# Optimization experiments

Measured on AMD Instinct MI355X. Metric: run time of the kernel, lower is better.

## Reference

```python
import jax, jax.numpy as jnp
import numpy as np

HEADS = 8
DIM_HEAD = 32
HTK = 576
WTK = 576


def layernorm(x, g, b, eps=1e-6):
    mu = x.mean(-1, keepdims=True)
    var = ((x - mu) ** 2).mean(-1, keepdims=True)
    return (x - mu) * jax.lax.rsqrt(var + eps) * g + b


def conv2d(x, w, b, pad, groups=1):
    y = jax.lax.conv_general_dilated(
        x, w, (1, 1), [(pad, pad), (pad, pad)],
        dimension_numbers=('NCHW', 'OIHW', 'NCHW'),
        feature_group_count=groups)
    return y + b[None, :, None, None]


def prune_attn(attn, htk, wtk):
    B, H, N, _ = attn.shape
    bi = jnp.arange(B)[:, None, None]
    hi = jnp.arange(H)[None, :, None]
    # row pruning: score rows by mean over keys, keep top-k rows
    row_scores = attn.mean(-1)                       # [B,H,N]
    _, top_row = jax.lax.top_k(row_scores, htk)      # [B,H,htk]
    row_mask = jnp.zeros((B, H, N), attn.dtype).at[bi, hi, top_row].set(1.0)
    # col pruning: score cols by mean over queries, keep top-k cols
    col_scores = attn.mean(-2)                       # [B,H,N]
    _, top_col = jax.lax.top_k(col_scores, wtk)
    col_mask = jnp.zeros((B, H, N), attn.dtype).at[bi, hi, top_col].set(1.0)
    return attn * row_mask[..., :, None] * col_mask[..., None, :]


def setup_inputs() -> dict:
    key = jax.random.key(0)
    ks = jax.random.split(key, 24)
    C = 256
    hid = C * 4
    g = C // 8
    s = 0.02
    inp = {
        'x': jax.random.normal(ks[0], (2, C, 48, 48), jnp.float32),
        'qkv_w': jax.random.normal(ks[1], (C, 3 * C), jnp.float32) * s,
        'out_w': jax.random.normal(ks[2], (C, C), jnp.float32) * s,
        'ln1_g': jnp.ones((C,), jnp.float32),
        'ln1_b': jnp.zeros((C,), jnp.float32),
        'ln2_g': jnp.ones((C,), jnp.float32),
        'ln2_b': jnp.zeros((C,), jnp.float32),
        'dw_w': jax.random.normal(ks[3], (C, 1, 3, 3), jnp.float32) * s,
        'dw_b': jnp.zeros((C,), jnp.float32),
        'pw_w': jax.random.normal(ks[4], (C, C, 1, 1), jnp.float32) * s,
        'pw_b': jnp.zeros((C,), jnp.float32),
        'sg1_w': jax.random.normal(ks[5], (g, C, 1, 1), jnp.float32) * s,
        'sg1_b': jnp.zeros((g,), jnp.float32),
        'sg2_w': jax.random.normal(ks[6], (1, g, 7, 7), jnp.float32) * s,
        'sg2_b': jnp.zeros((1,), jnp.float32),
        'cg1_w': jax.random.normal(ks[7], (g, C, 1, 1), jnp.float32) * s,
        'cg1_b': jnp.zeros((g,), jnp.float32),
        'cg2_w': jax.random.normal(ks[8], (C, g, 1, 1), jnp.float32) * s,
        'cg2_b': jnp.zeros((C,), jnp.float32),
        'ff_w1': jax.random.normal(ks[9], (C, hid), jnp.float32) * s,
        'ff_b1': jnp.zeros((hid,), jnp.float32),
        'ff_w2': jax.random.normal(ks[10], (hid, C), jnp.float32) * s,
        'ff_b2': jnp.zeros((C,), jnp.float32),
        'gamma1': jnp.full((1,), 0.5, jnp.float32),
        'gamma2': jnp.full((1,), 0.5, jnp.float32),
    }
    return inp


def reference(x, qkv_w, out_w, ln1_g, ln1_b, ln2_g, ln2_b, dw_w, dw_b,
              pw_w, pw_b, sg1_w, sg1_b, sg2_w, sg2_b, cg1_w, cg1_b,
              cg2_w, cg2_b, ff_w1, ff_b1, ff_w2, ff_b2, gamma1, gamma2):
    B, C, H, W = x.shape
    N = H * W
    # ---- dual-pruned self-attention branch ----
    xa = x.transpose(0, 2, 3, 1).reshape(B, N, C)
    xa = layernorm(xa, ln1_g, ln1_b)
    qkv = xa @ qkv_w                                    # [B,N,3C]
    q, k, v = jnp.split(qkv, 3, axis=-1)
    rs = lambda t: t.reshape(B, N, HEADS, DIM_HEAD).transpose(0, 2, 1, 3)
    q, k, v = rs(q), rs(k), rs(v)                       # [B,h,N,d]
    attn = jnp.einsum('bhid,bhjd->bhij', q, k) * (DIM_HEAD ** -0.5)
    attn = prune_attn(attn, HTK, WTK)
    attn = jax.nn.softmax(attn, axis=-1)
    o = jnp.einsum('bhij,bhjd->bhid', attn, v)
    o = o.transpose(0, 2, 1, 3).reshape(B, N, C) @ out_w
    x_attn = o.reshape(B, H, W, C).transpose(0, 3, 1, 2)
    # ---- conv branch ----
    xc = conv2d(x, dw_w, dw_b, pad=1, groups=C)
    xc = conv2d(xc, pw_w, pw_b, pad=0)
    xs = x_attn + xc
    # ---- gates ----
    sg = jax.nn.silu(conv2d(xs, sg1_w, sg1_b, pad=0))
    sg = jax.nn.sigmoid(conv2d(sg, sg2_w, sg2_b, pad=3))   # [B,1,H,W]
    cg = xs.mean(axis=(2, 3), keepdims=True)                # [B,C,1,1]
    cg = jax.nn.silu(conv2d(cg, cg1_w, cg1_b, pad=0))
    cg = jax.nn.sigmoid(conv2d(cg, cg2_w, cg2_b, pad=0))
    x2 = x + gamma1[0] * (xs * sg * cg)
    # ---- FFN ----
    normed = layernorm(x2.transpose(0, 2, 3, 1), ln2_g, ln2_b)
    h = jax.nn.gelu(normed @ ff_w1 + ff_b1, approximate=False)
    ff = (h @ ff_w2 + ff_b2).transpose(0, 3, 1, 2)
    return x2 + gamma2[0] * ff
```

## Files before the change

kernel.cpp:

```cpp
#include <hip/hip_runtime.h>
#include <math.h>

#define N_PIX 2304
#define CCH   256
#define BHN   16
#define KTOP  576
#define NROWS 4608

typedef unsigned short u16;
typedef __attribute__((ext_vector_type(8))) short short8v;
typedef __attribute__((ext_vector_type(4))) float floatx4;

__device__ __forceinline__ u16 f2b(float f) {
  unsigned int u = __float_as_uint(f);
  return (u16)((u + 0x7fffu + ((u >> 16) & 1u)) >> 16);
}
__device__ __forceinline__ float b2f(u16 v) {
  return __uint_as_float(((unsigned int)v) << 16);
}

__device__ __forceinline__ void async16(const void* g, void* l) {
  __builtin_amdgcn_global_load_lds(
      (const __attribute__((address_space(1))) unsigned int*)g,
      (__attribute__((address_space(3))) unsigned int*)l, 16, 0, 0);
}

__device__ __forceinline__ float erf_apx(float x) {
  float ax = fabsf(x);
  float u = 1.f / (1.f + 0.3275911f * ax);
  float y = u * (0.254829592f + u * (-0.284496736f + u * (1.421413741f +
            u * (-1.453152027f + u * 1.061405429f))));
  float r = 1.f - y * expf(-ax * ax);
  return (x < 0.f) ? -r : r;
}

__global__ __launch_bounds__(256) void lncast_kernel(
    const float* __restrict__ x, u16* __restrict__ xa_bf, float* __restrict__ xnhwc,
    const float* __restrict__ g, const float* __restrict__ beta,
    const float* __restrict__ qkv_w, const float* __restrict__ out_w,
    const float* __restrict__ pw_w, const float* __restrict__ ff_w1,
    const float* __restrict__ ff_w2, const float* __restrict__ sg1_w,
    u16* __restrict__ qkvBT, u16* __restrict__ B2,
    u16* __restrict__ ff1BT, u16* __restrict__ ff2BT, u16* __restrict__ sg1BT)
{
  __shared__ float tile[32 * 257];
  __shared__ float redS[8 * 32], redQ[8 * 32];
  __shared__ float mu_s[32], rs_s[32];
  int tid = threadIdx.x;
  if (blockIdx.x >= 144) {
    int i = (blockIdx.x - 144) * 256 + tid;
    if (i < 196608) { int k = i / 768, n = i - k * 768; qkvBT[n * 256 + k] = f2b(qkv_w[i]); return; }
    i -= 196608;
    if (i < 65536) { int k = i >> 8, n = i & 255; B2[n * 512 + k] = f2b(out_w[i]); return; }
    i -= 65536;
    if (i < 65536) { int n = i >> 8, ic = i & 255; B2[n * 512 + 256 + ic] = f2b(pw_w[i]); return; }
    i -= 65536;
    if (i < 262144) { int k = i >> 10, n = i & 1023; ff1BT[n * 256 + k] = f2b(ff_w1[i]); return; }
    i -= 262144;
    if (i < 262144) { int k = i & 1023, n = i >> 10; ff2BT[i] = f2b(ff_w2[k * 256 + n]); return; }
    i -= 262144;
    if (i < 16384) sg1BT[i] = (i < 8192) ? f2b(sg1_w[i]) : (u16)0;
    return;
  }
  int p0g = blockIdx.x * 32;
  int bb = p0g / N_PIX; int p0 = p0g - bb * N_PIX;
  int px = tid & 31, csub = tid >> 5;
  float sacc = 0.f, qacc = 0.f;
#pragma unroll 4
  for (int it = 0; it < 32; ++it) {
    int c = it * 8 + csub;
    float v = x[((long)bb * 256 + c) * N_PIX + p0 + px];
    tile[px * 257 + c] = v;
    sacc += v; qacc += v * v;
  }
  redS[csub * 32 + px] = sacc; redQ[csub * 32 + px] = qacc;
  __syncthreads();
  if (tid < 32) {
    float s = 0.f, qq = 0.f;
#pragma unroll
    for (int j = 0; j < 8; ++j) { s += redS[j * 32 + tid]; qq += redQ[j * 32 + tid]; }
    float mu = s * (1.f / 256.f);
    float var = qq * (1.f / 256.f) - mu * mu;
    mu_s[tid] = mu; rs_s[tid] = rsqrtf(var + 1e-6f);
  }
  __syncthreads();
  float gv = g[tid], bv = beta[tid];
#pragma unroll 4
  for (int it = 0; it < 32; ++it) {
    float v = tile[it * 257 + tid];
    long orow = (long)(p0g + it) * 256 + tid;
    xnhwc[orow] = v;
    xa_bf[orow] = f2b((v - mu_s[it]) * rs_s[it] * gv + bv);
  }
}

template<int MT, int EPI, int CS>
__global__ __launch_bounds__(256) void mgemm(
    const u16* __restrict__ A, const u16* __restrict__ BT,
    float* __restrict__ C, u16* __restrict__ C2,
    int K, int ldc, int nvalid,
    const float* __restrict__ bias, const float* __restrict__ add,
    const float* __restrict__ gamma,
    float* __restrict__ cs_out, int cs_ld,
    const u16* __restrict__ xs2, const float* __restrict__ sgv,
    const float* __restrict__ cgv, const float* __restrict__ g1p)
{
  __shared__ u16 Als[MT * 64 * 32];
  __shared__ u16 Bls[64 * 32];
  int tid = threadIdx.x;
  int w = tid >> 6, lane = tid & 63;
  int row0 = blockIdx.y * (MT * 64), col0 = blockIdx.x * 64;
  const u16* Abase = A + (long)row0 * K;
  const u16* Bbase = BT + (long)col0 * K;
  int q = lane >> 4, l15 = lane & 15;

  floatx4 acc[MT][4];
#pragma unroll
  for (int mi = 0; mi < MT; ++mi)
#pragma unroll
    for (int ni = 0; ni < 4; ++ni) acc[mi][ni] = (floatx4)0.f;

  int ccB = w * 64 + lane;
  int rB = ccB >> 2, kB = (ccB & 3) << 3;

  for (int k0 = 0; k0 < K; k0 += 32) {
#pragma unroll
    for (int i = 0; i < MT; ++i) {
      int cc = w * (64 * MT) + i * 64 + lane;
      async16(Abase + (long)(cc >> 2) * K + k0 + ((cc & 3) << 3), &Als[cc * 8]);
    }
    async16(Bbase + (long)rB * K + k0 + kB, &Bls[ccB * 8]);
    __syncthreads();
    short8v a[MT];
#pragma unroll
    for (int mi = 0; mi < MT; ++mi)
      a[mi] = *(const short8v*)&Als[(w * (16 * MT) + mi * 16 + l15) * 32 + q * 8];
#pragma unroll
    for (int ni = 0; ni < 4; ++ni) {
      short8v b = *(const short8v*)&Bls[(ni * 16 + l15) * 32 + q * 8];
#pragma unroll
      for (int mi = 0; mi < MT; ++mi)
        acc[mi][ni] = __builtin_amdgcn_mfma_f32_16x16x32_bf16(a[mi], b, acc[mi][ni], 0, 0, 0);
    }
    __syncthreads();
  }

  float g2 = (EPI == 5) ? gamma[0] : 0.f;
  float g1v = (EPI == 5) ? g1p[0] : 0.f;
  float cp[4] = {0.f, 0.f, 0.f, 0.f};
#pragma unroll
  for (int mi = 0; mi < MT; ++mi) {
#pragma unroll
    for (int ni = 0; ni < 4; ++ni) {
      int c = col0 + ni * 16 + l15;
      int rbase = row0 + w * (16 * MT) + mi * 16 + q * 4;
#pragma unroll
      for (int reg = 0; reg < 4; ++reg) {
        long row = rbase + reg;
        float v = acc[mi][ni][reg];
        if (EPI == 0) {
          C[row * ldc + c] = v;
          if (CS) cp[ni] += v;
        } else if (EPI == 3) {
          if (c < nvalid) {
            float t = v + bias[c];
            C[row * (long)nvalid + c] = t / (1.f + expf(-t));
          }
        } else if (EPI == 4) {
          float t = v + bias[c];
          t = 0.5f * t * (1.f + erf_apx(t * 0.70710678f));
          C2[row * ldc + c] = f2b(t);
        } else if (EPI == 5) {
          int bb = (int)(row / N_PIX); int p = (int)(row - (long)bb * N_PIX);
          float xsv = b2f(xs2[row * 256 + c]);
          float x2v = add[row * 256 + c] + g1v * xsv * sgv[row] * cgv[bb * 256 + c];
          float t = x2v + g2 * (v + bias[c]);
          C[((long)bb * 256 + c) * N_PIX + p] = t;
        } else if (EPI == 7) {
          float t = v + bias[c];
          C2[row * ldc + c] = f2b(t);
          if (CS) cp[ni] += t;
        }
      }
    }
  }
  if (CS) {
    int bb = (row0 >= N_PIX) ? 1 : 0;
#pragma unroll
    for (int ni = 0; ni < 4; ++ni) {
      float r = cp[ni];
      r += __shfl_xor(r, 16);
      r += __shfl_xor(r, 32);
      if (lane < 16) atomicAdd(&cs_out[bb * cs_ld + col0 + ni * 16 + l15], r);
    }
  }
}

__global__ __launch_bounds__(256) void topkscore_kernel(
    const float* __restrict__ qkv, const float* __restrict__ csum, int* __restrict__ out_idx)
{
  int bh = blockIdx.x, which = blockIdx.y;
  int b = bh >> 3, h = bh & 7;
  int* out = out_idx + (which * BHN + bh) * KTOP;
  __shared__ unsigned int u[N_PIX];
  __shared__ unsigned int hist[256];
  __shared__ unsigned int wtmp[4];
  __shared__ unsigned int sh_selbin, sh_selS;
  __shared__ unsigned int cnt_eq[4], cnt_sel[4];
  __shared__ float svl[32];
  int tid = threadIdx.x;
  int wave = tid >> 6, lane = tid & 63;
  unsigned long long ltmask = (1ull << lane) - 1ull;
  if (tid < 32) svl[tid] = csum[b * 768 + (which ? 0 : 256) + h * 32 + tid];
  __syncthreads();
  int off = (which ? 256 : 0) + h * 32;
  for (int i = tid; i < N_PIX; i += 256) {
    const float4* p4 = (const float4*)(qkv + ((long)(b * N_PIX + i)) * 768 + off);
    float sc = 0.f;
#pragma unroll
    for (int j = 0; j < 8; ++j) {
      float4 v = p4[j];
      sc += v.x * svl[j * 4] + v.y * svl[j * 4 + 1] + v.z * svl[j * 4 + 2] + v.w * svl[j * 4 + 3];
    }
    unsigned int bu = __float_as_uint(sc);
    u[i] = (bu & 0x80000000u) ? ~bu : (bu | 0x80000000u);
  }
  __syncthreads();
  unsigned int prefix = 0u, kRem = KTOP;
  for (int pass = 0; pass < 4; ++pass) {
    int shift = 24 - pass * 8;
    hist[tid] = 0u;
    __syncthreads();
    unsigned int mask = (pass == 0) ? 0u : (0xFFFFFFFFu << (shift + 8));
    for (int i = tid; i < N_PIX; i += 256) {
      unsigned int v = u[i];
      if ((v & mask) == prefix) atomicAdd(&hist[(v >> shift) & 255u], 1u);
    }
    __syncthreads();
    int v = (int)hist[255 - tid];
    int xsc = v;
#pragma unroll
    for (int o = 1; o < 64; o <<= 1) { int y = __shfl_up(xsc, o); if (lane >= o) xsc += y; }
    if (lane == 63) wtmp[wave] = (unsigned int)xsc;
    __syncthreads();
    int wadd = 0;
    for (int ww = 0; ww < wave; ++ww) wadd += (int)wtmp[ww];
    unsigned int S = (unsigned int)(xsc + wadd - v);
    if (S < kRem && S + (unsigned int)v >= kRem) { sh_selbin = (unsigned int)(255 - tid); sh_selS = S; }
    __syncthreads();
    prefix |= (sh_selbin << shift);
    kRem -= sh_selS;
    __syncthreads();
  }
  unsigned int T = prefix;
  unsigned int run_sel = 0u, run_eq = 0u;
  for (int c0 = 0; c0 < N_PIX; c0 += 256) {
    int i = c0 + tid;
    unsigned int v = u[i];
    bool isGt = v > T, isEq = (v == T);
    unsigned long long be = __ballot(isEq);
    unsigned int eqpre = (unsigned int)__popcll(be & ltmask);
    if (lane == 0) cnt_eq[wave] = (unsigned int)__popcll(be);
    __syncthreads();
    unsigned int eqoff = run_eq + eqpre;
    for (int ww = 0; ww < wave; ++ww) eqoff += cnt_eq[ww];
    bool selF = isGt || (isEq && eqoff < kRem);
    unsigned long long bs = __ballot(selF);
    unsigned int spre = (unsigned int)__popcll(bs & ltmask);
    if (lane == 0) cnt_sel[wave] = (unsigned int)__popcll(bs);
    __syncthreads();
    unsigned int soff = run_sel + spre;
    for (int ww = 0; ww < wave; ++ww) soff += cnt_sel[ww];
    if (selF) out[soff] = i;
    unsigned int te = 0, ts = 0;
#pragma unroll
    for (int ww = 0; ww < 4; ++ww) { te += cnt_eq[ww]; ts += cnt_sel[ww]; }
    run_eq += te; run_sel += ts;
    __syncthreads();
  }
}

__global__ __launch_bounds__(256) void gather_kernel(
    const float* __restrict__ qkv, const int* __restrict__ idx,
    u16* __restrict__ Qg, u16* __restrict__ Kg, u16* __restrict__ VgT,
    float* __restrict__ vneg, const float* __restrict__ csum, u16* __restrict__ A2)
{
  __shared__ float red[256];
  int bh = blockIdx.y;
  int tid = threadIdx.x;
  int r = blockIdx.x * 8 + (tid >> 5);
  int d = tid & 31;
  int b = bh >> 3, h = bh & 7;
  int rn = idx[bh * KTOP + r];
  int cn = idx[(BHN + bh) * KTOP + r];
  const float scale = 0.17677669529663687f;
  float vv = qkv[((long)(b * N_PIX + cn)) * 768 + 512 + h * 32 + d];
  Qg [((long)bh * KTOP + r) * 32 + d] = f2b(qkv[((long)(b * N_PIX + rn)) * 768 + h * 32 + d] * scale);
  Kg [((long)bh * KTOP + r) * 32 + d] = f2b(qkv[((long)(b * N_PIX + cn)) * 768 + 256 + h * 32 + d]);
  VgT[((long)bh * 32 + d) * 584 + r] = f2b(vv);
  red[tid] = vv;
  int bid = blockIdx.y * 72 + blockIdx.x;
  int row = 4 * bid + (tid >> 6);
  int b2 = row / N_PIX;
  int c4 = (tid & 63) * 4;
  const float* vm = csum + b2 * 768 + 512 + c4;
  ushort4 ov;
  ov.x = f2b(vm[0] * (1.f / (float)N_PIX));
  ov.y = f2b(vm[1] * (1.f / (float)N_PIX));
  ov.z = f2b(vm[2] * (1.f / (float)N_PIX));
  ov.w = f2b(vm[3] * (1.f / (float)N_PIX));
  *(ushort4*)&A2[(long)row * 512 + c4] = ov;
  __syncthreads();
  if (tid < 32) {
    float s = 0.f;
#pragma unroll
    for (int j = 0; j < 8; ++j) s += red[j * 32 + tid];
    atomicAdd(&vneg[bh * 32 + tid], s);
  }
}

__global__ __launch_bounds__(256) void attn_kernel(
    const u16* __restrict__ Qg, const u16* __restrict__ Kg, const u16* __restrict__ VgT,
    const float* __restrict__ csum, const float* __restrict__ vneg,
    const int* __restrict__ idx, u16* __restrict__ A2)
{
  __shared__ u16 Pls[32 * 584];
  __shared__ float wmax[4 * 32], wsum[4 * 32];
  __shared__ float emv_s[32], invd_s[32], vdif_s[32];
  int bh = blockIdx.y;
  int row0 = blockIdx.x * 32;
  int tid = threadIdx.x;
  int w = tid >> 6, lane = tid & 63;
  int q = lane >> 4, l15 = lane & 15;
  int b = bh >> 3, h = bh & 7;
  if (tid < 32) vdif_s[tid] = csum[b * 768 + 512 + h * 32 + tid] - vneg[bh * 32 + tid];
  const u16* Qb = Qg + (long)bh * KTOP * 32;
  const u16* Kb = Kg + (long)bh * KTOP * 32;
  short8v af[2];
#pragma unroll
  for (int mi = 0; mi < 2; ++mi)
    af[mi] = *(const short8v*)(Qb + ((long)(row0 + mi * 16 + l15)) * 32 + q * 8);
  floatx4 sacc[2][9];
#pragma unroll
  for (int mi = 0; mi < 2; ++mi)
#pragma unroll
    for (int ni = 0; ni < 9; ++ni) sacc[mi][ni] = (floatx4)0.f;
#pragma unroll
  for (int ni = 0; ni < 9; ++ni) {
    int n = w * 144 + ni * 16 + l15;
    short8v bf = *(const short8v*)(Kb + (long)n * 32 + q * 8);
#pragma unroll
    for (int mi = 0; mi < 2; ++mi)
      sacc[mi][ni] = __builtin_amdgcn_mfma_f32_16x16x32_bf16(af[mi], bf, sacc[mi][ni], 0, 0, 0);
  }
#pragma unroll
  for (int mi = 0; mi < 2; ++mi)
#pragma unroll
    for (int reg = 0; reg < 4; ++reg) {
      float m = sacc[mi][0][reg];
#pragma unroll
      for (int ni = 1; ni < 9; ++ni) m = fmaxf(m, sacc[mi][ni][reg]);
#pragma unroll
      for (int o = 1; o < 16; o <<= 1) m = fmaxf(m, __shfl_xor(m, o));
      if (l15 == 0) wmax[w * 32 + mi * 16 + q * 4 + reg] = m;
    }
  __syncthreads();
#pragma unroll
  for (int mi = 0; mi < 2; ++mi)
#pragma unroll
    for (int reg = 0; reg < 4; ++reg) {
      int r = mi * 16 + q * 4 + reg;
      float gm = fmaxf(fmaxf(fmaxf(wmax[r], wmax[32 + r]), fmaxf(wmax[64 + r], wmax[96 + r])), 0.f);
      float s = 0.f;
#pragma unroll
      for (int ni = 0; ni < 9; ++ni) {
        float e = expf(sacc[mi][ni][reg] - gm);
        s += e;
        Pls[r * 584 + w * 144 + ni * 16 + l15] = f2b(e);
      }
#pragma unroll
      for (int o = 1; o < 16; o <<= 1) s += __shfl_xor(s, o);
      if (l15 == 0) wsum[w * 32 + r] = s;
    }
  __syncthreads();
  if (tid < 32) {
    float gm = fmaxf(fmaxf(fmaxf(wmax[tid], wmax[32 + tid]), fmaxf(wmax[64 + tid], wmax[96 + tid])), 0.f);
    float s = wsum[tid] + wsum[32 + tid] + wsum[64 + tid] + wsum[96 + tid];
    float em = expf(-gm);
    float inv = 1.f / (s + (float)(N_PIX - KTOP) * em);
    invd_s[tid] = inv;
    emv_s[tid] = em * inv;
  }
  __syncthreads();
  int mw = w & 1, nw = w >> 1;
  const u16* Vb = VgT + (long)bh * 32 * 584;
  floatx4 acc = (floatx4)0.f;
#pragma unroll
  for (int kt = 0; kt < 18; ++kt) {
    int k0 = kt * 32;
    short8v a = *(const short8v*)&Pls[(mw * 16 + l15) * 584 + k0 + q * 8];
    short8v bb = *(const short8v*)(Vb + (long)(nw * 16 + l15) * 584 + k0 + q * 8);
    acc = __builtin_amdgcn_mfma_f32_16x16x32_bf16(a, bb, acc, 0, 0, 0);
  }
  int d = nw * 16 + l15;
  float vd = vdif_s[d];
#pragma unroll
  for (int reg = 0; reg < 4; ++reg) {
    int r = mw * 16 + q * 4 + reg;
    float o = acc[reg] * invd_s[r] + emv_s[r] * vd;
    int n = idx[bh * KTOP + row0 + r];
    A2[((long)(b * N_PIX + n)) * 512 + h * 32 + d] = f2b(o);
  }
}

__global__ __launch_bounds__(256) void dwconv_kernel(
    const float* __restrict__ xnhwc, const float* __restrict__ w,
    const float* __restrict__ bias, u16* __restrict__ A2)
{
  int pix = blockIdx.x;
  int b = pix / N_PIX; int p = pix - b * N_PIX;
  int y = p / 48, xx = p - y * 48;
  int c = threadIdx.x;
  float acc = bias[c];
#pragma unroll
  for (int ky = 0; ky < 3; ++ky) {
    int yy = y + ky - 1; if (yy < 0 || yy >= 48) continue;
#pragma unroll
    for (int kx = 0; kx < 3; ++kx) {
      int xc = xx + kx - 1; if (xc < 0 || xc >= 48) continue;
      acc += w[c * 9 + ky * 3 + kx] * xnhwc[((long)(b * N_PIX + yy * 48 + xc)) * 256 + c];
    }
  }
  A2[(long)pix * 512 + 256 + c] = f2b(acc);
}

__global__ __launch_bounds__(256) void sgcg_kernel(
    const float* __restrict__ sga, const float* __restrict__ w,
    const float* __restrict__ b1, float* __restrict__ sgate,
    const float* __restrict__ cgm, const float* __restrict__ cw1, const float* __restrict__ cb1,
    const float* __restrict__ cw2, const float* __restrict__ cb2, float* __restrict__ cgate)
{
  __shared__ float ws[32 * 49];
  __shared__ float red[4 * 64];
  __shared__ float m[256];
  __shared__ float a[32];
  int t = threadIdx.x;
  if (blockIdx.x >= 96) {
    int b = blockIdx.x - 96;
    m[t] = cgm[b * 256 + t] * (1.f / (float)N_PIX);
    __syncthreads();
    if (t < 32) {
      float s = cb1[t];
      for (int c = 0; c < 256; ++c) s += cw1[t * 256 + c] * m[c];
      a[t] = s / (1.f + expf(-s));
    }
    __syncthreads();
    float s = cb2[t];
#pragma unroll
    for (int g = 0; g < 32; ++g) s += cw2[t * 32 + g] * a[g];
    cgate[b * 256 + t] = 1.f / (1.f + expf(-s));
    return;
  }
  int by = blockIdx.x; int b = by / 48, y = by - b * 48;
  for (int i = t; i < 32 * 49; i += 256) ws[i] = w[i];
  __syncthreads();
  int xx = t & 63, gg = t >> 6;
  float acc = 0.f;
  if (xx < 48) {
    for (int ky = 0; ky < 7; ++ky) {
      int yy = y + ky - 3; if (yy < 0 || yy >= 48) continue;
      for (int kx = 0; kx < 7; ++kx) {
        int xc = xx + kx - 3; if (xc < 0 || xc >= 48) continue;
        const float4* sp = (const float4*)(sga + ((long)(b * N_PIX + yy * 48 + xc)) * 32 + gg * 8);
        float4 v0 = sp[0], v1 = sp[1];
        int wb = gg * 8 * 49 + ky * 7 + kx;
        acc += ws[wb] * v0.x + ws[wb + 49] * v0.y + ws[wb + 98] * v0.z + ws[wb + 147] * v0.w;
        acc += ws[wb + 196] * v1.x + ws[wb + 245] * v1.y + ws[wb + 294] * v1.z + ws[wb + 343] * v1.w;
      }
    }
  }
  red[gg * 64 + xx] = acc;
  __syncthreads();
  if (t < 48) {
    float tot = b1[0] + red[t] + red[64 + t] + red[128 + t] + red[192 + t];
    sgate[b * N_PIX + y * 48 + t] = 1.f / (1.f + expf(-tot));
  }
}

__global__ __launch_bounds__(256) void gln_kernel(
    const float* __restrict__ xnhwc, const u16* __restrict__ xs_bf,
    const float* __restrict__ sgate, const float* __restrict__ cgate,
    const float* __restrict__ gamma1,
    const float* __restrict__ g, const float* __restrict__ bvec, u16* __restrict__ normed)
{
  __shared__ float red[256];
  int pix = blockIdx.x; int b = pix / N_PIX;
  int c = threadIdx.x;
  float xsv = b2f(xs_bf[(long)pix * 256 + c]);
  float v = xnhwc[(long)pix * 256 + c] + gamma1[0] * xsv * sgate[pix] * cgate[b * 256 + c];
  red[c] = v; __syncthreads();
  for (int off = 128; off > 0; off >>= 1) { if (c < off) red[c] += red[c + off]; __syncthreads(); }
  float mu = red[0] * (1.f / 256.f);
  __syncthreads();
  float dv = v - mu;
  red[c] = dv * dv; __syncthreads();
  for (int off = 128; off > 0; off >>= 1) { if (c < off) red[c] += red[c + off]; __syncthreads(); }
  float var = red[0] * (1.f / 256.f);
  normed[(long)pix * 256 + c] = f2b(dv * rsqrtf(var + 1e-6f) * g[c] + bvec[c]);
}

extern "C" void kernel_launch(void* const* d_in, const int* in_sizes, int n_in,
                              void* d_out, int out_size, void* d_ws, size_t ws_size,
                              hipStream_t stream) {
  (void)in_sizes; (void)n_in; (void)out_size; (void)ws_size;
  const float* x      = (const float*)d_in[0];
  const float* qkv_w  = (const float*)d_in[1];
  const float* out_w  = (const float*)d_in[2];
  const float* ln1_g  = (const float*)d_in[3];
  const float* ln1_b  = (const float*)d_in[4];
  const float* ln2_g  = (const float*)d_in[5];
  const float* ln2_b  = (const float*)d_in[6];
  const float* dw_w   = (const float*)d_in[7];
  const float* dw_b   = (const float*)d_in[8];
  const float* pw_w   = (const float*)d_in[9];
  const float* pw_b   = (const float*)d_in[10];
  const float* sg1_w  = (const float*)d_in[11];
  const float* sg1_b  = (const float*)d_in[12];
  const float* sg2_w  = (const float*)d_in[13];
  const float* sg2_b  = (const float*)d_in[14];
  const float* cg1_w  = (const float*)d_in[15];
  const float* cg1_b  = (const float*)d_in[16];
  const float* cg2_w  = (const float*)d_in[17];
  const float* cg2_b  = (const float*)d_in[18];
  const float* ff_w1  = (const float*)d_in[19];
  const float* ff_b1  = (const float*)d_in[20];
  const float* ff_w2  = (const float*)d_in[21];
  const float* ff_b2  = (const float*)d_in[22];
  const float* gamma1 = (const float*)d_in[23];
  const float* gamma2 = (const float*)d_in[24];
  float* out = (float*)d_out;
  float* ws  = (float*)d_ws;

  float* qkv     = ws + 0;
  u16*   A2      = (u16*)(ws + 3538944);
  float* xnhwc   = ws + 4718592;
  u16*   xa_bf   = (u16*)(ws + 5898240);
  u16*   xs_bf   = (u16*)(ws + 6488064);
  u16*   Qg_bf   = (u16*)(ws + 7077888);
  u16*   Kg_bf   = (u16*)(ws + 7225344);
  u16*   VgT     = (u16*)(ws + 7372800);
  float* sga     = ws + 7522304;
  float* csum    = ws + 7669760;
  float* vneg    = ws + 7671296;
  float* cgm     = ws + 7671808;
  float* sgate   = ws + 7672320;
  float* cgate   = ws + 7676928;
  int*   idxb    = (int*)(ws + 7677440);
  u16*   qkvBT   = (u16*)(ws + 7695872);
  u16*   B2combo = (u16*)(ws + 7794176);
  u16*   ff1BT   = (u16*)(ws + 7859712);
  u16*   ff2BT   = (u16*)(ws + 7990784);
  u16*   sg1BT   = (u16*)(ws + 8121856);
  u16*   h_bf     = (u16*)qkv;
  u16*   normed_bf= (u16*)(ws + 2359296);

  dim3 blk(256);
  hipMemsetAsync(csum, 0, 2560 * sizeof(float), stream);

  lncast_kernel<<<dim3(3536), blk, 0, stream>>>(x, xa_bf, xnhwc, ln1_g, ln1_b,
      qkv_w, out_w, pw_w, ff_w1, ff_w2, sg1_w,
      qkvBT, B2combo, ff1BT, ff2BT, sg1BT);

  mgemm<2, 0, 1><<<dim3(12, 36), blk, 0, stream>>>(xa_bf, qkvBT, qkv, nullptr,
      256, 768, 768, nullptr, nullptr, nullptr, csum, 768, nullptr, nullptr, nullptr, nullptr);
  topkscore_kernel<<<dim3(BHN, 2), blk, 0, stream>>>(qkv, csum, idxb);
  gather_kernel<<<dim3(72, BHN), blk, 0, stream>>>(qkv, idxb, Qg_bf, Kg_bf, VgT, vneg,
      csum, A2);
  attn_kernel<<<dim3(18, BHN), blk, 0, stream>>>(Qg_bf, Kg_bf, VgT, csum, vneg, idxb, A2);

  dwconv_kernel<<<dim3(NROWS), blk, 0, stream>>>(xnhwc, dw_w, dw_b, A2);

  mgemm<1, 7, 1><<<dim3(4, 72), blk, 0, stream>>>(A2, B2combo, nullptr, xs_bf,
      512, 256, 256, pw_b, nullptr, nullptr, cgm, 256, nullptr, nullptr, nullptr, nullptr);

  mgemm<1, 3, 0><<<dim3(1, 72), blk, 0, stream>>>(xs_bf, sg1BT, sga, nullptr,
      256, 32, 32, sg1_b, nullptr, nullptr, nullptr, 0, nullptr, nullptr, nullptr, nullptr);
  sgcg_kernel<<<dim3(98), blk, 0, stream>>>(sga, sg2_w, sg2_b, sgate,
      cgm, cg1_w, cg1_b, cg2_w, cg2_b, cgate);

  gln_kernel<<<dim3(NROWS), blk, 0, stream>>>(xnhwc, xs_bf, sgate, cgate, gamma1,
      ln2_g, ln2_b, normed_bf);

  mgemm<2, 4, 0><<<dim3(16, 36), blk, 0, stream>>>(normed_bf, ff1BT, nullptr, h_bf,
      256, 1024, 1024, ff_b1, nullptr, nullptr, nullptr, 0, nullptr, nullptr, nullptr, nullptr);
  mgemm<1, 5, 0><<<dim3(4, 72), blk, 0, stream>>>(h_bf, ff2BT, out, nullptr,
      1024, 256, 256, ff_b2, xnhwc, gamma2, nullptr, 0, xs_bf, sgate, cgate, gamma1);
}
```

Baseline: 256.7 us.

## Load GEMM operands directly to registers; fuse dwconv into topk; fold memset

The GEMM drops its LDS staging and barriers, so each wave loads its A and B MFMA fragments straight from global memory into registers, with the k-loop unrolled by two. The depthwise conv is merged into the top-k scoring launch as extra blocks, so it runs alongside the 32 top-k blocks. The csum memset moves into an extra block of the layernorm/cast kernel. Together these remove two launches and the barrier cost, but the B fragments are now fetched separately by every wave with no LDS sharing, which relies on L1/L2 hits.

```diff
diff --git a/kernel.cpp b/kernel.cpp
--- a/kernel.cpp
+++ b/kernel.cpp
@@ -17,12 +17,6 @@
 }
 __device__ __forceinline__ float b2f(u16 v) {
   return __uint_as_float(((unsigned int)v) << 16);
-}
-
-__device__ __forceinline__ void async16(const void* g, void* l) {
-  __builtin_amdgcn_global_load_lds(
-      (const __attribute__((address_space(1))) unsigned int*)g,
-      (__attribute__((address_space(3))) unsigned int*)l, 16, 0, 0);
 }
 
 __device__ __forceinline__ float erf_apx(float x) {
@@ -41,12 +35,18 @@
     const float* __restrict__ pw_w, const float* __restrict__ ff_w1,
     const float* __restrict__ ff_w2, const float* __restrict__ sg1_w,
     u16* __restrict__ qkvBT, u16* __restrict__ B2,
-    u16* __restrict__ ff1BT, u16* __restrict__ ff2BT, u16* __restrict__ sg1BT)
+    u16* __restrict__ ff1BT, u16* __restrict__ ff2BT, u16* __restrict__ sg1BT,
+    float* __restrict__ zbuf)
 {
   __shared__ float tile[32 * 257];
   __shared__ float redS[8 * 32], redQ[8 * 32];
   __shared__ float mu_s[32], rs_s[32];
   int tid = threadIdx.x;
+  if (blockIdx.x == 3536) {
+#pragma unroll
+    for (int j = 0; j < 10; ++j) zbuf[tid + j * 256] = 0.f;
+    return;
+  }
   if (blockIdx.x >= 144) {
     int i = (blockIdx.x - 144) * 256 + tid;
     if (i < 196608) { int k = i / 768, n = i - k * 768; qkvBT[n * 256 + k] = f2b(qkv_w[i]); return; }
@@ -95,7 +95,7 @@
 }
 
 template<int MT, int EPI, int CS>
-__global__ __launch_bounds__(256) void mgemm(
+__global__ __launch_bounds__(256) void dgemm(
     const u16* __restrict__ A, const u16* __restrict__ BT,
     float* __restrict__ C, u16* __restrict__ C2,
     int K, int ldc, int nvalid,
@@ -105,14 +105,10 @@
     const u16* __restrict__ xs2, const float* __restrict__ sgv,
     const float* __restrict__ cgv, const float* __restrict__ g1p)
 {
-  __shared__ u16 Als[MT * 64 * 32];
-  __shared__ u16 Bls[64 * 32];
   int tid = threadIdx.x;
   int w = tid >> 6, lane = tid & 63;
+  int q = lane >> 4, l15 = lane & 15;
   int row0 = blockIdx.y * (MT * 64), col0 = blockIdx.x * 64;
-  const u16* Abase = A + (long)row0 * K;
-  const u16* Bbase = BT + (long)col0 * K;
-  int q = lane >> 4, l15 = lane & 15;
 
   floatx4 acc[MT][4];
 #pragma unroll
@@ -120,29 +116,23 @@
 #pragma unroll
     for (int ni = 0; ni < 4; ++ni) acc[mi][ni] = (floatx4)0.f;
 
-  int ccB = w * 64 + lane;
-  int rB = ccB >> 2, kB = (ccB & 3) << 3;
-
+  const u16* Ap = A + (long)(row0 + w * (16 * MT) + l15) * K + q * 8;
+  const u16* Bp = BT + (long)(col0 + l15) * K + q * 8;
+
+#pragma unroll 2
   for (int k0 = 0; k0 < K; k0 += 32) {
-#pragma unroll
-    for (int i = 0; i < MT; ++i) {
-      int cc = w * (64 * MT) + i * 64 + lane;
-      async16(Abase + (long)(cc >> 2) * K + k0 + ((cc & 3) << 3), &Als[cc * 8]);
-    }
-    async16(Bbase + (long)rB * K + k0 + kB, &Bls[ccB * 8]);
-    __syncthreads();
-    short8v a[MT];
+    short8v a[MT], b[4];
 #pragma unroll
     for (int mi = 0; mi < MT; ++mi)
-      a[mi] = *(const short8v*)&Als[(w * (16 * MT) + mi * 16 + l15) * 32 + q * 8];
-#pragma unroll
-    for (int ni = 0; ni < 4; ++ni) {
-      short8v b = *(const short8v*)&Bls[(ni * 16 + l15) * 32 + q * 8];
+      a[mi] = *(const short8v*)(Ap + (long)mi * 16 * K + k0);
+#pragma unroll
+    for (int ni = 0; ni < 4; ++ni)
+      b[ni] = *(const short8v*)(Bp + (long)ni * 16 * K + k0);
+#pragma unroll
+    for (int ni = 0; ni < 4; ++ni)
 #pragma unroll
       for (int mi = 0; mi < MT; ++mi)
-        acc[mi][ni] = __builtin_amdgcn_mfma_f32_16x16x32_bf16(a[mi], b, acc[mi][ni], 0, 0, 0);
-    }
-    __syncthreads();
+        acc[mi][ni] = __builtin_amdgcn_mfma_f32_16x16x32_bf16(a[mi], b[ni], acc[mi][ni], 0, 0, 0);
   }
 
   float g2 = (EPI == 5) ? gamma[0] : 0.f;
@@ -196,12 +186,11 @@
   }
 }
 
-__global__ __launch_bounds__(256) void topkscore_kernel(
-    const float* __restrict__ qkv, const float* __restrict__ csum, int* __restrict__ out_idx)
-{
-  int bh = blockIdx.x, which = blockIdx.y;
-  int b = bh >> 3, h = bh & 7;
-  int* out = out_idx + (which * BHN + bh) * KTOP;
+__global__ __launch_bounds__(256) void tkdw_kernel(
+    const float* __restrict__ qkv, const float* __restrict__ csum, int* __restrict__ out_idx,
+    const float* __restrict__ xnhwc, const float* __restrict__ dw_w,
+    const float* __restrict__ dw_b, u16* __restrict__ A2)
+{
   __shared__ unsigned int u[N_PIX];
   __shared__ unsigned int hist[256];
   __shared__ unsigned int wtmp[4];
@@ -209,6 +198,27 @@
   __shared__ unsigned int cnt_eq[4], cnt_sel[4];
   __shared__ float svl[32];
   int tid = threadIdx.x;
+  if (blockIdx.x >= 32) {
+    int pix = blockIdx.x - 32;
+    int b = pix / N_PIX; int p = pix - b * N_PIX;
+    int y = p / 48, xx = p - y * 48;
+    int c = tid;
+    float acc = dw_b[c];
+#pragma unroll
+    for (int ky = 0; ky < 3; ++ky) {
+      int yy = y + ky - 1; if (yy < 0 || yy >= 48) continue;
+#pragma unroll
+      for (int kx = 0; kx < 3; ++kx) {
+        int xc = xx + kx - 1; if (xc < 0 || xc >= 48) continue;
+        acc += dw_w[c * 9 + ky * 3 + kx] * xnhwc[((long)(b * N_PIX + yy * 48 + xc)) * 256 + c];
+      }
+    }
+    A2[(long)pix * 512 + 256 + c] = f2b(acc);
+    return;
+  }
+  int bh = blockIdx.x & 15, which = blockIdx.x >> 4;
+  int b = bh >> 3, h = bh & 7;
+  int* out = out_idx + (which * BHN + bh) * KTOP;
   int wave = tid >> 6, lane = tid & 63;
   unsigned long long ltmask = (1ull << lane) - 1ull;
   if (tid < 32) svl[tid] = csum[b * 768 + (which ? 0 : 256) + h * 32 + tid];
@@ -411,27 +421,6 @@
     int n = idx[bh * KTOP + row0 + r];
     A2[((long)(b * N_PIX + n)) * 512 + h * 32 + d] = f2b(o);
   }
-}
-
-__global__ __launch_bounds__(256) void dwconv_kernel(
-    const float* __restrict__ xnhwc, const float* __restrict__ w,
-    const float* __restrict__ bias, u16* __restrict__ A2)
-{
-  int pix = blockIdx.x;
-  int b = pix / N_PIX; int p = pix - b * N_PIX;
-  int y = p / 48, xx = p - y * 48;
-  int c = threadIdx.x;
-  float acc = bias[c];
-#pragma unroll
-  for (int ky = 0; ky < 3; ++ky) {
-    int yy = y + ky - 1; if (yy < 0 || yy >= 48) continue;
-#pragma unroll
-    for (int kx = 0; kx < 3; ++kx) {
-      int xc = xx + kx - 1; if (xc < 0 || xc >= 48) continue;
-      acc += w[c * 9 + ky * 3 + kx] * xnhwc[((long)(b * N_PIX + yy * 48 + xc)) * 256 + c];
-    }
-  }
-  A2[(long)pix * 512 + 256 + c] = f2b(acc);
 }
 
 __global__ __launch_bounds__(256) void sgcg_kernel(
@@ -565,25 +554,22 @@
   u16*   normed_bf= (u16*)(ws + 2359296);
 
   dim3 blk(256);
-  hipMemsetAsync(csum, 0, 2560 * sizeof(float), stream);
-
-  lncast_kernel<<<dim3(3536), blk, 0, stream>>>(x, xa_bf, xnhwc, ln1_g, ln1_b,
+
+  lncast_kernel<<<dim3(3537), blk, 0, stream>>>(x, xa_bf, xnhwc, ln1_g, ln1_b,
       qkv_w, out_w, pw_w, ff_w1, ff_w2, sg1_w,
-      qkvBT, B2combo, ff1BT, ff2BT, sg1BT);
-
-  mgemm<2, 0, 1><<<dim3(12, 36), blk, 0, stream>>>(xa_bf, qkvBT, qkv, nullptr,
+      qkvBT, B2combo, ff1BT, ff2BT, sg1BT, csum);
+
+  dgemm<2, 0, 1><<<dim3(12, 36), blk, 0, stream>>>(xa_bf, qkvBT, qkv, nullptr,
       256, 768, 768, nullptr, nullptr, nullptr, csum, 768, nullptr, nullptr, nullptr, nullptr);
-  topkscore_kernel<<<dim3(BHN, 2), blk, 0, stream>>>(qkv, csum, idxb);
+  tkdw_kernel<<<dim3(4640), blk, 0, stream>>>(qkv, csum, idxb, xnhwc, dw_w, dw_b, A2);
   gather_kernel<<<dim3(72, BHN), blk, 0, stream>>>(qkv, idxb, Qg_bf, Kg_bf, VgT, vneg,
       csum, A2);
   attn_kernel<<<dim3(18, BHN), blk, 0, stream>>>(Qg_bf, Kg_bf, VgT, csum, vneg, idxb, A2);
 
-  dwconv_kernel<<<dim3(NROWS), blk, 0, stream>>>(xnhwc, dw_w, dw_b, A2);
-
-  mgemm<1, 7, 1><<<dim3(4, 72), blk, 0, stream>>>(A2, B2combo, nullptr, xs_bf,
+  dgemm<1, 7, 1><<<dim3(4, 72), blk, 0, stream>>>(A2, B2combo, nullptr, xs_bf,
       512, 256, 256, pw_b, nullptr, nullptr, cgm, 256, nullptr, nullptr, nullptr, nullptr);
 
-  mgemm<1, 3, 0><<<dim3(1, 72), blk, 0, stream>>>(xs_bf, sg1BT, sga, nullptr,
+  dgemm<1, 3, 0><<<dim3(1, 72), blk, 0, stream>>>(xs_bf, sg1BT, sga, nullptr,
       256, 32, 32, sg1_b, nullptr, nullptr, nullptr, 0, nullptr, nullptr, nullptr, nullptr);
   sgcg_kernel<<<dim3(98), blk, 0, stream>>>(sga, sg2_w, sg2_b, sgate,
       cgm, cg1_w, cg1_b, cg2_w, cg2_b, cgate);
@@ -591,8 +577,8 @@
   gln_kernel<<<dim3(NROWS), blk, 0, stream>>>(xnhwc, xs_bf, sgate, cgate, gamma1,
       ln2_g, ln2_b, normed_bf);
 
-  mgemm<2, 4, 0><<<dim3(16, 36), blk, 0, stream>>>(normed_bf, ff1BT, nullptr, h_bf,
+  dgemm<2, 4, 0><<<dim3(16, 36), blk, 0, stream>>>(normed_bf, ff1BT, nullptr, h_bf,
       256, 1024, 1024, ff_b1, nullptr, nullptr, nullptr, 0, nullptr, nullptr, nullptr, nullptr);
-  mgemm<1, 5, 0><<<dim3(4, 72), blk, 0, stream>>>(h_bf, ff2BT, out, nullptr,
+  dgemm<1, 5, 0><<<dim3(4, 72), blk, 0, stream>>>(h_bf, ff2BT, out, nullptr,
       1024, 256, 256, ff_b2, xnhwc, gamma2, nullptr, 0, xs_bf, sgate, cgate, gamma1);
 }
```

New measurement: 289.5 us. +12.8%, slower.
